# Performance work log

Hardware: AMD Instinct MI355X
Metric: run time of the kernel (lower is better)

The kernel has to match this reference:

```python
import jax, jax.numpy as jnp
import numpy as np

B, C1, C2, K, H, W = 2, 256, 256, 3, 64, 64
PAD = 1
EPS = 1e-5
K2 = K * K
OUT_OFF = 3 * K2  # deform_groups=1: 2*k2 offset channels + k2 mask channels


def setup_inputs() -> dict:
    key = jax.random.key(0)
    ks = jax.random.split(key, 8)
    x = jax.random.normal(ks[0], (B, C1, H, W), jnp.float32)
    # small scale so predicted offsets stay within a few pixels (realistic trained regime)
    w_off = jax.random.normal(ks[1], (OUT_OFF, C1, 3, 3), jnp.float32) * 0.01
    b_off = jax.random.normal(ks[2], (OUT_OFF,), jnp.float32) * 0.01
    w_dcn = jax.random.normal(ks[3], (C2, C1, K, K), jnp.float32) / np.sqrt(C1 * K2).astype(np.float32)
    gamma = 1.0 + 0.1 * jax.random.normal(ks[4], (C2,), jnp.float32)
    beta = 0.1 * jax.random.normal(ks[5], (C2,), jnp.float32)
    run_mean = 0.1 * jax.random.normal(ks[6], (C2,), jnp.float32)
    run_var = jax.random.uniform(ks[7], (C2,), jnp.float32, minval=0.5, maxval=1.5)
    return {"x": x, "w_off": w_off, "b_off": b_off, "w_dcn": w_dcn,
            "gamma": gamma, "beta": beta, "run_mean": run_mean, "run_var": run_var}


def _dcnv2_bn_silu(x, w_off, b_off, w_dcn, gamma, beta, run_mean, run_var):
    # offset/mask predictor: plain 3x3 conv, stride 1, pad 1
    om = jax.lax.conv_general_dilated(x, w_off, (1, 1), [(PAD, PAD), (PAD, PAD)])
    om = om + b_off[None, :, None, None]  # [B, 27, H, W]
    # mmcv channel layout: (dy, dx) interleaved per kernel tap, then mask
    offset = om[:, :2 * K2].reshape(B, K2, 2, H, W)
    mask = jax.nn.sigmoid(om[:, 2 * K2:3 * K2])  # [B, K2, H, W]
    dy, dx = offset[:, :, 0], offset[:, :, 1]     # [B, K2, H, W]

    ki = jnp.arange(K)
    tap_y = jnp.repeat(ki, K)  # [K2]
    tap_x = jnp.tile(ki, K)    # [K2]
    base_y = jnp.arange(H)[None, None, :, None] - PAD + tap_y[None, :, None, None]
    base_x = jnp.arange(W)[None, None, None, :] - PAD + tap_x[None, :, None, None]
    py = base_y.astype(x.dtype) + dy  # [B, K2, H, W] sampling rows
    px = base_x.astype(x.dtype) + dx  # [B, K2, H, W] sampling cols

    y0f = jnp.floor(py)
    x0f = jnp.floor(px)
    ly = (py - y0f)[:, None]  # [B, 1, K2, H, W]
    lx = (px - x0f)[:, None]
    y0 = y0f.astype(jnp.int32)
    x0 = x0f.astype(jnp.int32)

    x_flat = x.reshape(B, C1, H * W)

    def gather(yi, xi):
        valid = ((yi >= 0) & (yi < H) & (xi >= 0) & (xi < W)).astype(x.dtype)
        idx = jnp.clip(yi, 0, H - 1) * W + jnp.clip(xi, 0, W - 1)  # [B, K2, H, W]
        v = jnp.take_along_axis(x_flat, idx.reshape(B, 1, -1), axis=2)
        return v.reshape(B, C1, K2, H, W) * valid[:, None]

    v00 = gather(y0, x0)
    v01 = gather(y0, x0 + 1)
    v10 = gather(y0 + 1, x0)
    v11 = gather(y0 + 1, x0 + 1)
    vals = (v00 * (1 - ly) * (1 - lx) + v01 * (1 - ly) * lx
            + v10 * ly * (1 - lx) + v11 * ly * lx)
    vals = vals * mask[:, None]  # modulated

    out = jnp.einsum('bckhw,ock->bohw', vals, w_dcn.reshape(C2, C1, K2))

    # BatchNorm (inference, running stats) + SiLU
    inv = gamma / jnp.sqrt(run_var + EPS)
    y = out * inv[None, :, None, None] + (beta - run_mean * inv)[None, :, None, None]
    return y * jax.nn.sigmoid(y)


def reference(x, w_off, b_off, w_dcn, gamma, beta, run_mean, run_var):
    return _dcnv2_bn_silu(x, w_off, b_off, w_dcn, gamma, beta, run_mean, run_var)
```

## Files before the change

### kernel.cpp

```cpp
#include <hip/hip_runtime.h>
#include <hip/hip_bf16.h>
#include <math.h>

typedef __bf16 bf16x8 __attribute__((ext_vector_type(8)));
typedef float  f32x4  __attribute__((ext_vector_type(4)));

#define BB 2
#define C1 256
#define C2 256
#define HH 64
#define WW 64
#define HW 4096
#define OCH 27
#define EPSV 1e-5f

#define WBF_OFF  0u
#define WOFF_OFF 1179648u
#define XT_OFF   1327104u

__global__ __launch_bounds__(256) void prep_kernel(
    const float* __restrict__ x, const float* __restrict__ w_dcn,
    const float* __restrict__ w_off, __bf16* __restrict__ xT,
    __bf16* __restrict__ wbfS, __bf16* __restrict__ woffS)
{
    __shared__ __bf16 tile[64][72];
    __shared__ __bf16 lw[16][584];
    const int bi = blockIdx.x, tid = threadIdx.x;

    if (bi < 512) {
        const int b = bi >> 8;
        const int ht = (bi & 255) >> 2;
        const int ct = bi & 3;
        const int hw_l = tid & 63, cg = tid >> 6;
        const float* src = x + ((size_t)(b * 256 + ct * 64 + cg * 16) << 12)
                             + ht * 64 + hw_l;
        #pragma unroll
        for (int i = 0; i < 16; i++)
            tile[hw_l][cg * 16 + i] = (__bf16)src[(size_t)i << 12];
        __syncthreads();
        const int hw_o = tid >> 2, cq = tid & 3;
        __bf16* dst = xT + ((size_t)(b * HW + ht * 64 + hw_o) << 8)
                         + ct * 64 + cq * 16;
        *(bf16x8*)dst       = *(const bf16x8*)&tile[hw_o][cq * 16];
        *(bf16x8*)(dst + 8) = *(const bf16x8*)&tile[hw_o][cq * 16 + 8];
    } else if (bi < 576) {
        const int b2 = bi - 512;
        const int nb = b2 >> 2, qtr = b2 & 3;
        #pragma unroll
        for (int ii = 0; ii < 9; ii++) {
            int m = tid + 256 * ii;
            int base = m * 4;
            int o_l = base / 576;
            int f = base - o_l * 576;
            float4 v = *(const float4*)(w_dcn
                + (size_t)(nb * 16 + o_l) * 2304 + qtr * 576 + f);
            lw[o_l][f]     = (__bf16)v.x;
            lw[o_l][f + 1] = (__bf16)v.y;
            lw[o_l][f + 2] = (__bf16)v.z;
            lw[o_l][f + 3] = (__bf16)v.w;
        }
        __syncthreads();
        for (int p = tid; p < 1152; p += 256) {
            int lane = p & 63, seg = p >> 6;
            int tap = seg >> 1, ks = seg & 1;
            int kb = tap * 4 + qtr;
            int o_l = lane & 15, kq = (lane >> 4) & 3;
            bf16x8 v;
            #pragma unroll
            for (int j = 0; j < 8; j++)
                v[j] = lw[o_l][(ks * 32 + kq * 8 + j) * 9 + tap];
            *(bf16x8*)(wbfS
                + ((size_t)(((kb * 2 + ks) * 16 + nb) * 64 + lane)) * 8) = v;
        }
    } else {
        int t = (bi - 576) * 256 + tid;
        int l = t & 63;
        int nf = (t >> 6) & 1;
        int ks = (t >> 7) & 1;
        int kb = t >> 8;
        int o = nf * 16 + (l & 15);
        int kq = (l >> 4) & 3;
        bf16x8 v;
        #pragma unroll
        for (int j = 0; j < 8; j++) {
            int K = kb * 64 + ks * 32 + kq * 8 + j;
            v[j] = (o < OCH) ? (__bf16)w_off[o * 2304 + (K & 255) * 9 + (K >> 8)]
                             : (__bf16)0.f;
        }
        *(bf16x8*)(woffS + (size_t)t * 8) = v;
    }
}

union SU {
    float sD[8][16][33];
    float sC[4][16][132];
};

__global__ __launch_bounds__(512, 4) void fused_kernel(
    const __bf16* __restrict__ xT, const __bf16* __restrict__ wbfS,
    const __bf16* __restrict__ woffS, const float* __restrict__ b_off,
    const float* __restrict__ gamma, const float* __restrict__ beta,
    const float* __restrict__ rmean, const float* __restrict__ rvar,
    float* __restrict__ out)
{
    __shared__ SU u;
    __shared__ float  sOm[32][16];
    __shared__ int4   sO[9][16];
    __shared__ float4 sW[9][16];

    const int tid = threadIdx.x, wv = tid >> 6, lane = tid & 63;
    const int g = (blockIdx.x & 7) * 64 + (blockIdx.x >> 3);
    const int pixBase = g * 16;
    const int b = pixBase >> 12;
    const int hwBase = pixBase & 4095;
    const int h = hwBase >> 6, w0 = hwBase & 63;
    const int n15 = lane & 15, q4 = lane >> 4;

    const int cc  = wv >> 1;
    const int ksw = wv & 1;
    const char* xb = (const char*)xT + ((size_t)b << 12) * 512;
    const int chOffB = (cc * 64 + ksw * 32 + q4 * 8) * 2;

    {
        f32x4 acc2[2];
        acc2[0] = (f32x4){0.f, 0.f, 0.f, 0.f};
        acc2[1] = (f32x4){0.f, 0.f, 0.f, 0.f};

        #pragma unroll
        for (int k = 0; k < 9; k++) {
            const int kb = k * 4 + cc;
            const int kh = k / 3, kw = k % 3;
            const int hh = h + kh - 1;
            const int ww = w0 + n15 + kw - 1;
            const bool valid = (hh >= 0) && (hh < HH) && (ww >= 0) && (ww < WW);
            const int hc = min(max(hh, 0), HH - 1);
            const int wc = min(max(ww, 0), WW - 1);
            bf16x8 af = *(const bf16x8*)(xb + (size_t)(hc * WW + wc) * 512
                                            + chOffB);
            if (!valid) {
                #pragma unroll
                for (int j = 0; j < 8; j++) af[j] = (__bf16)0.f;
            }
            #pragma unroll
            for (int nf = 0; nf < 2; nf++) {
                bf16x8 bfr = *(const bf16x8*)(woffS
                    + ((size_t)(((kb * 2 + ksw) * 2 + nf) * 64 + lane)) * 8);
                acc2[nf] = __builtin_amdgcn_mfma_f32_16x16x32_bf16(
                    af, bfr, acc2[nf], 0, 0, 0);
            }
        }
        #pragma unroll
        for (int nf = 0; nf < 2; nf++)
            #pragma unroll
            for (int r = 0; r < 4; r++)
                u.sD[wv][q4 * 4 + r][nf * 16 + n15] = acc2[nf][r];
    }
    __syncthreads();
    if (tid < OCH * 16) {
        int oc = tid >> 4, p = tid & 15;
        float s = b_off[oc];
        #pragma unroll
        for (int w = 0; w < 8; w++) s += u.sD[w][p][oc];
        sOm[oc][p] = s;
    }
    __syncthreads();

    if (tid < 144) {
        int k = tid >> 4, p = tid & 15;
        float dy = sOm[2 * k][p];
        float dx = sOm[2 * k + 1][p];
        float mm = sOm[18 + k][p];
        mm = 1.f / (1.f + __expf(-mm));
        float py = (float)(h - 1 + k / 3) + dy;
        float px = (float)(w0 + p - 1 + k % 3) + dx;
        float y0f = floorf(py), x0f = floorf(px);
        float ly = py - y0f, lx = px - x0f;
        int y0 = (int)y0f, x0 = (int)x0f;
        int yc0 = min(max(y0, 0), HH - 1),     yc1 = min(max(y0 + 1, 0), HH - 1);
        int xc0 = min(max(x0, 0), WW - 1),     xc1 = min(max(x0 + 1, 0), WW - 1);
        float vy0 = (y0 >= 0 && y0 < HH) ? 1.f : 0.f;
        float vy1 = (y0 + 1 >= 0 && y0 + 1 < HH) ? 1.f : 0.f;
        float vx0 = (x0 >= 0 && x0 < WW) ? 1.f : 0.f;
        float vx1 = (x0 + 1 >= 0 && x0 + 1 < WW) ? 1.f : 0.f;
        sO[k][p] = (int4){(yc0 * WW + xc0) * 512, (yc0 * WW + xc1) * 512,
                          (yc1 * WW + xc0) * 512, (yc1 * WW + xc1) * 512};
        sW[k][p] = (float4){(1.f - ly) * (1.f - lx) * vy0 * vx0 * mm,
                            (1.f - ly) * lx         * vy0 * vx1 * mm,
                            ly         * (1.f - lx) * vy1 * vx0 * mm,
                            ly         * lx         * vy1 * vx1 * mm};
    }
    __syncthreads();

    f32x4 acc[16];
    #pragma unroll
    for (int j = 0; j < 16; j++) acc[j] = (f32x4){0.f, 0.f, 0.f, 0.f};

    for (int k = 0; k < 9; k++) {
        const int kb = k * 4 + cc;
        const int4   O = sO[k][n15];
        const float4 W = sW[k][n15];
        const char* base = xb + chOffB;

        bf16x8 c00 = *(const bf16x8*)(base + O.x);
        bf16x8 c01 = *(const bf16x8*)(base + O.y);
        bf16x8 c10 = *(const bf16x8*)(base + O.z);
        bf16x8 c11 = *(const bf16x8*)(base + O.w);
        bf16x8 af;
        #pragma unroll
        for (int j = 0; j < 8; j++) {
            float v = W.x * (float)c00[j] + W.y * (float)c01[j]
                    + W.z * (float)c10[j] + W.w * (float)c11[j];
            af[j] = (__bf16)v;
        }

        #pragma unroll
        for (int hf = 0; hf < 2; hf++) {
            bf16x8 bfr[8];
            #pragma unroll
            for (int nb = 0; nb < 8; nb++)
                bfr[nb] = *(const bf16x8*)(wbfS
                    + ((size_t)(((kb * 2 + ksw) * 16 + hf * 8 + nb) * 64 + lane)) * 8);
            #pragma unroll
            for (int nb = 0; nb < 8; nb++)
                acc[hf * 8 + nb] = __builtin_amdgcn_mfma_f32_16x16x32_bf16(
                    af, bfr[nb], acc[hf * 8 + nb], 0, 0, 0);
        }
    }

    #pragma unroll
    for (int pass = 0; pass < 2; pass++) {
        if (wv < 4) {
            #pragma unroll
            for (int nb = 0; nb < 8; nb++)
                #pragma unroll
                for (int r = 0; r < 4; r++)
                    u.sC[wv][q4 * 4 + r][nb * 16 + n15] = acc[pass * 8 + nb][r];
        }
        __syncthreads();
        if (wv >= 4) {
            #pragma unroll
            for (int nb = 0; nb < 8; nb++)
                #pragma unroll
                for (int r = 0; r < 4; r++)
                    u.sC[wv - 4][q4 * 4 + r][nb * 16 + n15] += acc[pass * 8 + nb][r];
        }
        __syncthreads();

        const int px = tid & 15, og = tid >> 4;
        #pragma unroll
        for (int ii = 0; ii < 4; ii++) {
            int col = og * 4 + ii;
            int o = pass * 128 + col;
            float s = u.sC[0][px][col] + u.sC[1][px][col]
                    + u.sC[2][px][col] + u.sC[3][px][col];
            float inv = gamma[o] * rsqrtf(rvar[o] + EPSV);
            float sh = beta[o] - rmean[o] * inv;
            float y = s * inv + sh;
            out[(size_t)((b * C2 + o) << 12) + hwBase + px]
                = y * (1.f / (1.f + __expf(-y)));
        }
        __syncthreads();
    }
}

extern "C" void kernel_launch(void* const* d_in, const int* in_sizes, int n_in,
                              void* d_out, int out_size, void* d_ws, size_t ws_size,
                              hipStream_t stream) {
    const float* x      = (const float*)d_in[0];
    const float* w_off  = (const float*)d_in[1];
    const float* b_off  = (const float*)d_in[2];
    const float* w_dcn  = (const float*)d_in[3];
    const float* gamma  = (const float*)d_in[4];
    const float* beta   = (const float*)d_in[5];
    const float* rmean  = (const float*)d_in[6];
    const float* rvar   = (const float*)d_in[7];
    float* out = (float*)d_out;

    char* ws = (char*)d_ws;
    __bf16* wbfS  = (__bf16*)(ws + WBF_OFF);
    __bf16* woffS = (__bf16*)(ws + WOFF_OFF);
    __bf16* xT    = (__bf16*)(ws + XT_OFF);

    prep_kernel<<<612, 256, 0, stream>>>(x, w_dcn, w_off, xT, wbfS, woffS);
    fused_kernel<<<512, 512, 0, stream>>>(xT, wbfS, woffS, b_off,
                                          gamma, beta, rmean, rvar, out);
}
```

Baseline: 123.0 us.

## Process 32 pixels per block to reuse weight fragments across two pixel tiles

```diff
diff --git a/kernel.cpp b/kernel.cpp
--- a/kernel.cpp
+++ b/kernel.cpp
@@ -92,11 +92,11 @@
 }
 
 union SU {
-    float sD[8][16][33];
-    float sC[4][16][132];
+    float sD[8][2][16][33];
+    float sC[4][32][133];
 };
 
-__global__ __launch_bounds__(512, 4) void fused_kernel(
+__global__ __launch_bounds__(512, 2) void fused_kernel(
     const __bf16* __restrict__ xT, const __bf16* __restrict__ wbfS,
     const __bf16* __restrict__ woffS, const float* __restrict__ b_off,
     const float* __restrict__ gamma, const float* __restrict__ beta,
@@ -104,13 +104,13 @@
     float* __restrict__ out)
 {
     __shared__ SU u;
-    __shared__ float  sOm[32][16];
-    __shared__ int4   sO[9][16];
-    __shared__ float4 sW[9][16];
+    __shared__ float  sOm[32][33];
+    __shared__ int4   sO[9][32];
+    __shared__ float4 sW[9][32];
 
     const int tid = threadIdx.x, wv = tid >> 6, lane = tid & 63;
-    const int g = (blockIdx.x & 7) * 64 + (blockIdx.x >> 3);
-    const int pixBase = g * 16;
+    const int g = (blockIdx.x & 7) * 32 + (blockIdx.x >> 3);
+    const int pixBase = g * 32;
     const int b = pixBase >> 12;
     const int hwBase = pixBase & 4095;
     const int h = hwBase >> 6, w0 = hwBase & 63;
@@ -122,51 +122,63 @@
     const int chOffB = (cc * 64 + ksw * 32 + q4 * 8) * 2;
 
     {
-        f32x4 acc2[2];
-        acc2[0] = (f32x4){0.f, 0.f, 0.f, 0.f};
-        acc2[1] = (f32x4){0.f, 0.f, 0.f, 0.f};
+        f32x4 acc2[2][2];
+        #pragma unroll
+        for (int nf = 0; nf < 2; nf++)
+            #pragma unroll
+            for (int t = 0; t < 2; t++)
+                acc2[nf][t] = (f32x4){0.f, 0.f, 0.f, 0.f};
 
         #pragma unroll
         for (int k = 0; k < 9; k++) {
             const int kb = k * 4 + cc;
             const int kh = k / 3, kw = k % 3;
             const int hh = h + kh - 1;
-            const int ww = w0 + n15 + kw - 1;
-            const bool valid = (hh >= 0) && (hh < HH) && (ww >= 0) && (ww < WW);
             const int hc = min(max(hh, 0), HH - 1);
-            const int wc = min(max(ww, 0), WW - 1);
-            bf16x8 af = *(const bf16x8*)(xb + (size_t)(hc * WW + wc) * 512
+            const bool vy = (hh >= 0) && (hh < HH);
+            bf16x8 af[2];
+            #pragma unroll
+            for (int t = 0; t < 2; t++) {
+                const int ww = w0 + t * 16 + n15 + kw - 1;
+                const bool valid = vy && (ww >= 0) && (ww < WW);
+                const int wc = min(max(ww, 0), WW - 1);
+                af[t] = *(const bf16x8*)(xb + (size_t)(hc * WW + wc) * 512
                                             + chOffB);
-            if (!valid) {
-                #pragma unroll
-                for (int j = 0; j < 8; j++) af[j] = (__bf16)0.f;
+                if (!valid) {
+                    #pragma unroll
+                    for (int j = 0; j < 8; j++) af[t][j] = (__bf16)0.f;
+                }
             }
             #pragma unroll
             for (int nf = 0; nf < 2; nf++) {
                 bf16x8 bfr = *(const bf16x8*)(woffS
                     + ((size_t)(((kb * 2 + ksw) * 2 + nf) * 64 + lane)) * 8);
-                acc2[nf] = __builtin_amdgcn_mfma_f32_16x16x32_bf16(
-                    af, bfr, acc2[nf], 0, 0, 0);
+                #pragma unroll
+                for (int t = 0; t < 2; t++)
+                    acc2[nf][t] = __builtin_amdgcn_mfma_f32_16x16x32_bf16(
+                        af[t], bfr, acc2[nf][t], 0, 0, 0);
             }
         }
         #pragma unroll
         for (int nf = 0; nf < 2; nf++)
             #pragma unroll
-            for (int r = 0; r < 4; r++)
-                u.sD[wv][q4 * 4 + r][nf * 16 + n15] = acc2[nf][r];
+            for (int t = 0; t < 2; t++)
+                #pragma unroll
+                for (int r = 0; r < 4; r++)
+                    u.sD[wv][t][q4 * 4 + r][nf * 16 + n15] = acc2[nf][t][r];
     }
     __syncthreads();
-    if (tid < OCH * 16) {
-        int oc = tid >> 4, p = tid & 15;
+    for (int t2 = tid; t2 < OCH * 32; t2 += 512) {
+        int oc = t2 >> 5, p = t2 & 31;
         float s = b_off[oc];
         #pragma unroll
-        for (int w = 0; w < 8; w++) s += u.sD[w][p][oc];
+        for (int w = 0; w < 8; w++) s += u.sD[w][p >> 4][p & 15][oc];
         sOm[oc][p] = s;
     }
     __syncthreads();
 
-    if (tid < 144) {
-        int k = tid >> 4, p = tid & 15;
+    if (tid < 288) {
+        int k = tid >> 5, p = tid & 31;
         float dy = sOm[2 * k][p];
         float dx = sOm[2 * k + 1][p];
         float mm = sOm[18 + k][p];
@@ -191,26 +203,36 @@
     }
     __syncthreads();
 
-    f32x4 acc[16];
+    f32x4 acc[2][16];
     #pragma unroll
-    for (int j = 0; j < 16; j++) acc[j] = (f32x4){0.f, 0.f, 0.f, 0.f};
-
+    for (int t = 0; t < 2; t++)
+        #pragma unroll
+        for (int j = 0; j < 16; j++) acc[t][j] = (f32x4){0.f, 0.f, 0.f, 0.f};
+
+    const char* base = xb + chOffB;
     for (int k = 0; k < 9; k++) {
         const int kb = k * 4 + cc;
-        const int4   O = sO[k][n15];
-        const float4 W = sW[k][n15];
-        const char* base = xb + chOffB;
-
-        bf16x8 c00 = *(const bf16x8*)(base + O.x);
-        bf16x8 c01 = *(const bf16x8*)(base + O.y);
-        bf16x8 c10 = *(const bf16x8*)(base + O.z);
-        bf16x8 c11 = *(const bf16x8*)(base + O.w);
-        bf16x8 af;
+        const int4   O0 = sO[k][n15],      O1 = sO[k][16 + n15];
+        const float4 W0 = sW[k][n15],      W1 = sW[k][16 + n15];
+
+        bf16x8 a00 = *(const bf16x8*)(base + O0.x);
+        bf16x8 a01 = *(const bf16x8*)(base + O0.y);
+        bf16x8 a10 = *(const bf16x8*)(base + O0.z);
+        bf16x8 a11 = *(const bf16x8*)(base + O0.w);
+        bf16x8 b00 = *(const bf16x8*)(base + O1.x);
+        bf16x8 b01 = *(const bf16x8*)(base + O1.y);
+        bf16x8 b10 = *(const bf16x8*)(base + O1.z);
+        bf16x8 b11 = *(const bf16x8*)(base + O1.w);
+
+        bf16x8 af0, af1;
         #pragma unroll
         for (int j = 0; j < 8; j++) {
-            float v = W.x * (float)c00[j] + W.y * (float)c01[j]
-                    + W.z * (float)c10[j] + W.w * (float)c11[j];
-            af[j] = (__bf16)v;
+            float v0 = W0.x * (float)a00[j] + W0.y * (float)a01[j]
+                     + W0.z * (float)a10[j] + W0.w * (float)a11[j];
+            float v1 = W1.x * (float)b00[j] + W1.y * (float)b01[j]
+                     + W1.z * (float)b10[j] + W1.w * (float)b11[j];
+            af0[j] = (__bf16)v0;
+            af1[j] = (__bf16)v1;
         }
 
         #pragma unroll
@@ -221,9 +243,12 @@
                 bfr[nb] = *(const bf16x8*)(wbfS
                     + ((size_t)(((kb * 2 + ksw) * 16 + hf * 8 + nb) * 64 + lane)) * 8);
             #pragma unroll
-            for (int nb = 0; nb < 8; nb++)
-                acc[hf * 8 + nb] = __builtin_amdgcn_mfma_f32_16x16x32_bf16(
-                    af, bfr[nb], acc[hf * 8 + nb], 0, 0, 0);
+            for (int nb = 0; nb < 8; nb++) {
+                acc[0][hf * 8 + nb] = __builtin_amdgcn_mfma_f32_16x16x32_bf16(
+                    af0, bfr[nb], acc[0][hf * 8 + nb], 0, 0, 0);
+                acc[1][hf * 8 + nb] = __builtin_amdgcn_mfma_f32_16x16x32_bf16(
+                    af1, bfr[nb], acc[1][hf * 8 + nb], 0, 0, 0);
+            }
         }
     }
 
@@ -231,25 +256,31 @@
     for (int pass = 0; pass < 2; pass++) {
         if (wv < 4) {
             #pragma unroll
-            for (int nb = 0; nb < 8; nb++)
+            for (int t = 0; t < 2; t++)
                 #pragma unroll
-                for (int r = 0; r < 4; r++)
-                    u.sC[wv][q4 * 4 + r][nb * 16 + n15] = acc[pass * 8 + nb][r];
+                for (int nb = 0; nb < 8; nb++)
+                    #pragma unroll
+                    for (int r = 0; r < 4; r++)
+                        u.sC[wv][t * 16 + q4 * 4 + r][nb * 16 + n15]
+                            = acc[t][pass * 8 + nb][r];
         }
         __syncthreads();
         if (wv >= 4) {
             #pragma unroll
-            for (int nb = 0; nb < 8; nb++)
+            for (int t = 0; t < 2; t++)
                 #pragma unroll
-                for (int r = 0; r < 4; r++)
-                    u.sC[wv - 4][q4 * 4 + r][nb * 16 + n15] += acc[pass * 8 + nb][r];
-        }
-        __syncthreads();
-
-        const int px = tid & 15, og = tid >> 4;
-        #pragma unroll
-        for (int ii = 0; ii < 4; ii++) {
-            int col = og * 4 + ii;
+                for (int nb = 0; nb < 8; nb++)
+                    #pragma unroll
+                    for (int r = 0; r < 4; r++)
+                        u.sC[wv - 4][t * 16 + q4 * 4 + r][nb * 16 + n15]
+                            += acc[t][pass * 8 + nb][r];
+        }
+        __syncthreads();
+
+        const int px = tid & 31, og = tid >> 5;
+        #pragma unroll
+        for (int ii = 0; ii < 8; ii++) {
+            int col = og * 8 + ii;
             int o = pass * 128 + col;
             float s = u.sC[0][px][col] + u.sC[1][px][col]
                     + u.sC[2][px][col] + u.sC[3][px][col];
@@ -282,6 +313,6 @@
     __bf16* xT    = (__bf16*)(ws + XT_OFF);
 
     prep_kernel<<<612, 256, 0, stream>>>(x, w_dcn, w_off, xT, wbfS, woffS);
-    fused_kernel<<<512, 512, 0, stream>>>(xT, wbfS, woffS, b_off,
+    fused_kernel<<<256, 512, 0, stream>>>(xT, wbfS, woffS, b_off,
                                           gamma, beta, rmean, rvar, out);
 }
```

Result: no change. 121.1 us (-1.5%).
